# Kernel tuning notes

Hardware: AMD Instinct MI355X
Metric: run time of the kernel (lower is better)

## Reference

```python
import jax, jax.numpy as jnp
from jax import lax
import numpy as np

EPS = 1e-5

def _quant(w):
    # BitNet-style binarization: sign(w) scaled by mean(|w|), with STE (identity grad)
    alpha = jnp.mean(jnp.abs(w))
    wq = jnp.sign(w) * alpha
    return w + lax.stop_gradient(wq - w)

def _bn(x, gamma, beta, axes):
    mean = jnp.mean(x, axis=axes, keepdims=True)
    var = jnp.var(x, axis=axes, keepdims=True)
    shape = [1] * x.ndim
    shape[1] = x.shape[1]
    return (x - mean) * lax.rsqrt(var + EPS) * gamma.reshape(shape) + beta.reshape(shape)

def _conv(x, w):
    return lax.conv_general_dilated(x, w, window_strides=(1, 1), padding=((1, 1), (1, 1)),
                                    dimension_numbers=('NCHW', 'OIHW', 'NCHW'))

def _maxpool2(x):
    return lax.reduce_window(x, -jnp.inf, lax.max, (1, 1, 2, 2), (1, 1, 2, 2), 'VALID')

def setup_inputs() -> dict:
    key = jax.random.key(0)
    ks = jax.random.split(key, 5)
    return {
        'x': jax.random.normal(ks[0], (1024, 3, 32, 32), jnp.float32),
        'w1': jax.random.normal(ks[1], (64, 3, 3, 3), jnp.float32) * 0.1,
        'g1': jnp.ones((64,), jnp.float32), 'b1': jnp.zeros((64,), jnp.float32),
        'w2': jax.random.normal(ks[2], (128, 64, 3, 3), jnp.float32) * 0.05,
        'g2': jnp.ones((128,), jnp.float32), 'b2': jnp.zeros((128,), jnp.float32),
        'wfc1': jax.random.normal(ks[3], (256, 8192), jnp.float32) * 0.02,
        'g3': jnp.ones((256,), jnp.float32), 'b3': jnp.zeros((256,), jnp.float32),
        'wfc2': jax.random.normal(ks[4], (10, 256), jnp.float32) * 0.1,
    }

def reference(x, w1, g1, b1, w2, g2, b2, wfc1, g3, b3, wfc2):
    h = _conv(x, _quant(w1))                 # [B,64,32,32]
    h = _maxpool2(jax.nn.relu(_bn(h, g1, b1, (0, 2, 3))))  # [B,64,16,16]
    h = _conv(h, _quant(w2))                 # [B,128,16,16]
    h = _maxpool2(jax.nn.relu(_bn(h, g2, b2, (0, 2, 3))))  # [B,128,8,8]
    h = h.reshape(h.shape[0], -1)            # [B,8192]
    h = h @ _quant(wfc1).T                   # [B,256]
    h = jax.nn.relu(_bn(h, g3, b3, (0,)))
    return h @ _quant(wfc2).T                # [B,10]
```

## Files before the change

### kernel.cpp

```cpp
#include <hip/hip_runtime.h>
#include <stdint.h>

typedef unsigned short u16;
typedef unsigned int u32;
typedef __attribute__((ext_vector_type(8))) short s8v;
typedef __attribute__((ext_vector_type(4))) float f4v;
typedef __attribute__((ext_vector_type(8))) u16 u16x8;
typedef __attribute__((ext_vector_type(4))) u16 u16x4;

__device__ __forceinline__ float bf2f(u16 u){
  union { u32 i; float f; } v; v.i = ((u32)u) << 16; return v.f;
}
__device__ __forceinline__ u16 f2bf(float f){
  union { float f; u32 i; } v; v.f = f;
  u32 i = v.i;
  return (u16)((i + 0x7fffu + ((i >> 16) & 1u)) >> 16);
}
__device__ __forceinline__ float sgnf(float w){
  return (w > 0.f) ? 1.f : ((w < 0.f) ? -1.f : 0.f);
}
__device__ __forceinline__ u16 sgn_bf(float w){
  return (w > 0.f) ? (u16)0x3F80 : ((w < 0.f) ? (u16)0xBF80 : (u16)0);
}

#define GLL16(gaddr, laddr) __builtin_amdgcn_global_load_lds( \
    (const __attribute__((address_space(1))) void*)(gaddr),   \
    (__attribute__((address_space(3))) void*)(laddr), 16, 0, 0)


__global__ __launch_bounds__(256) void k_gen(const float* __restrict__ w1, const float* __restrict__ w2,
                                             const float* __restrict__ wfc2, const float* __restrict__ wfc1,
                                             u16* __restrict__ qw1b, u16* __restrict__ qw2b,
                                             float* __restrict__ qwfc2, u16* __restrict__ qfc1b,
                                             float* __restrict__ absum){
  __shared__ u16 tile[128*72];
  int t = threadIdx.x;
  if (blockIdx.x < 306){
    int i = blockIdx.x * 256 + t;
    if (i < 73728){
      int j = i & 7, lane = (i >> 3) & 63, fid = i >> 9;
      int s = fid >> 4, ks = (fid >> 3) & 1, nt = fid & 7;
      int co = (lane & 15)*8 + nt;
      int c_pos = ks*32 + (lane >> 4)*8 + j;
      int c6 = c_pos & 63;
      int c_orig = ((c6 & 3) << 4) + (c6 >> 2);
      qw2b[i] = sgn_bf(w2[((size_t)co*64 + c_orig)*9 + s]);
    } else if (i < 73728 + 2048){
      int i3 = i - 73728;
      int j = i3 & 7, lane = (i3 >> 3) & 63, nt = i3 >> 9;
      int co = nt*16 + (lane & 15);
      int k = (lane >> 4)*8 + j;
      qw1b[i3] = (k < 27) ? sgn_bf(w1[co*27 + k]) : (u16)0;
    } else {
      int i4 = i - (73728 + 2048);
      float wv = wfc2[i4];
      qwfc2[i4] = sgnf(wv);
      float av = fabsf(wv);
      #pragma unroll
      for (int off = 32; off > 0; off >>= 1) av += __shfl_xor(av, off);
      if ((t & 63) == 0) atomicAdd(absum + 3, av);
    }
  } else {
    int co = blockIdx.x - 306;
    const float4* src = (const float4*)(wfc1 + (size_t)co*8192);
    #pragma unroll
    for (int p = 0; p < 8; ++p){
      int k4 = t + p*256;
      float4 v = src[k4];
      int c = k4 >> 4, px = (k4 & 15)*4;
      u16* d = tile + c*72 + px;
      d[0] = sgn_bf(v.x); d[1] = sgn_bf(v.y); d[2] = sgn_bf(v.z); d[3] = sgn_bf(v.w);
    }
    __syncthreads();
    int co4 = co >> 4, co15 = co & 15;
    #pragma unroll
    for (int p = 0; p < 4; ++p){
      int m = t + p*256;
      int px = m >> 4, jj = m & 15;
      int kstep = px*4 + (jj >> 2), l16 = jj & 3;
      u16x8 o;
      #pragma unroll
      for (int u = 0; u < 8; ++u) o[u] = tile[(jj*8 + u)*72 + px];
      *(u16x8*)(qfc1b + ((size_t)(kstep*16 + co4)*512 + (l16*16 + co15)*8)) = o;
    }
  }
}

__global__ __launch_bounds__(256) void k_conv1m(const float* __restrict__ x, const u16* __restrict__ qw1b,
                                                u16* __restrict__ p1raw,
                                                float* __restrict__ gs, float* __restrict__ gq){
  __shared__ __align__(8) u16 xs[3*34*36];
  __shared__ float ls1[64], ls2[64];
  int n = blockIdx.x, t = threadIdx.x;
  if (t < 64){ ls1[t] = 0.f; ls2[t] = 0.f; }
  for (int i = t; i < 1836; i += 256) ((u32*)xs)[i] = 0u;
  __syncthreads();
  const float4* xg = (const float4*)(x + (size_t)n * 3072);
  for (int i = t; i < 768; i += 256){
    float4 v = xg[i];
    int ci = i >> 8, rem = i & 255, y = rem >> 3, xq = (rem & 7) * 4;
    int base = ci*1224 + (y+1)*36 + 2 + xq;
    *(u32*)(xs + base)     = (u32)f2bf(v.x) | ((u32)f2bf(v.y) << 16);
    *(u32*)(xs + base + 2) = (u32)f2bf(v.z) | ((u32)f2bf(v.w) << 16);
  }
  int w = t >> 6, lane = t & 63, l15 = lane & 15, q = lane >> 4;
  int koff[8]; u32 kmsk[8];
  #pragma unroll
  for (int j = 0; j < 8; ++j){
    int k = q*8 + j;
    int d9 = (k*57) >> 9;
    int r9 = k - d9*9;
    int d3 = (r9*11) >> 5;
    int r3 = r9 - d3*3;
    koff[j] = d9*1224 + d3*36 + r3;
    kmsk[j] = (k < 27) ? 0xffffu : 0u;
  }
  const s8v* bp = (const s8v*)qw1b;
  s8v bf[4];
  #pragma unroll
  for (int nt = 0; nt < 4; ++nt) bf[nt] = bp[nt*64 + lane];
  u16* p1img = p1raw + (size_t)n * 16384;
  float s1v[4], s2v[4];
  #pragma unroll
  for (int nt = 0; nt < 4; ++nt){ s1v[nt] = 0.f; s2v[nt] = 0.f; }
  __syncthreads();
  for (int chunk = 0; chunk < 4; ++chunk){
    #pragma unroll
    for (int i = 0; i < 4; ++i){
      int tl = w*4 + i;
      int r = tl*16 + l15;
      int g = (chunk*256 + r) >> 2, s = r & 3;
      int iy = 2*(g >> 4) + (s >> 1), ix = 2*(g & 15) + (s & 1);
      const u16* xb = xs + iy*36 + ix + 1;
      u32 pk2[4];
      #pragma unroll
      for (int kk = 0; kk < 4; ++kk){
        u32 lo = (u32)xb[koff[2*kk]]     & kmsk[2*kk];
        u32 hi = (u32)xb[koff[2*kk + 1]] & kmsk[2*kk + 1];
        pk2[kk] = lo | (hi << 16);
      }
      s8v av;
      ((u32*)&av)[0] = pk2[0]; ((u32*)&av)[1] = pk2[1];
      ((u32*)&av)[2] = pk2[2]; ((u32*)&av)[3] = pk2[3];
      int go = chunk*64 + tl*4 + q;
      u16x4 pk;
      #pragma unroll
      for (int nt = 0; nt < 4; ++nt){
        f4v c = (f4v)(0.0f);
        c = __builtin_amdgcn_mfma_f32_16x16x32_bf16(av, bf[nt], c, 0, 0, 0);
        s1v[nt] += c[0] + c[1] + c[2] + c[3];
        s2v[nt] += c[0]*c[0] + c[1]*c[1] + c[2]*c[2] + c[3]*c[3];
        float pm = fmaxf(fmaxf(c[0], c[1]), fmaxf(c[2], c[3]));
        pk[nt] = f2bf(pm);
      }
      *(u16x4*)(p1img + go*64 + l15*4) = pk;
    }
  }
  #pragma unroll
  for (int nt = 0; nt < 4; ++nt){
    s1v[nt] += __shfl_xor(s1v[nt], 16); s1v[nt] += __shfl_xor(s1v[nt], 32);
    s2v[nt] += __shfl_xor(s2v[nt], 16); s2v[nt] += __shfl_xor(s2v[nt], 32);
  }
  if (q == 0){
    #pragma unroll
    for (int nt = 0; nt < 4; ++nt){
      atomicAdd(&ls1[l15*4 + nt], s1v[nt]);
      atomicAdd(&ls2[l15*4 + nt], s2v[nt]);
    }
  }
  __syncthreads();
  if (t < 64){
    atomicAdd(gs + t, ls1[t]);
    atomicAdd(gq + t, ls2[t]);
  }
}

__global__ __launch_bounds__(512, 4) void k_conv2m(const u16* __restrict__ p1raw, const u16* __restrict__ qw2b,
                                                   const float* __restrict__ s1, const float* __restrict__ q1,
                                                   const float* __restrict__ g1, const float* __restrict__ b1,
                                                   u16* __restrict__ p2raw,
                                                   float* __restrict__ gs, float* __restrict__ gq){
  __shared__ __align__(16) u16 img[288*64];
  __shared__ __align__(16) u16 bstage[3][4096];
  int n = blockIdx.x, t = threadIdx.x;
  int c0 = (t & 7) * 8;
  float scv[8], biv[8];
  #pragma unroll
  for (int j = 0; j < 8; ++j){
    int cp = c0 + j;
    int corig = ((cp & 3) << 4) + (cp >> 2);
    float m = s1[cp] * (1.f/1048576.f);
    float var = q1[cp] * (1.f/1048576.f) - m*m;
    float sc = g1[corig] * rsqrtf(var + 1e-5f);
    scv[j] = sc; biv[j] = b1[corig] - m*sc;
  }
  if (t < 256){
    int cl = t >> 7, y = (t >> 3) & 15, unit = t & 7;
    int px = y*18 + cl*17;
    int su = unit ^ (px & 7);
    *(u16x8*)(img + px*64 + su*8) = (u16x8)(u16)0;
  }
  const u16* src = p1raw + (size_t)n * 16384;
  #pragma unroll
  for (int i = 0; i < 4; ++i){
    int id = i*512 + t;
    int p0 = id >> 3, unit = id & 7;
    int y = p0 >> 4, xq = p0 & 15;
    int px = y*18 + xq + 1;
    int su = unit ^ (px & 7);
    u16x8 v = *(const u16x8*)(src + id*8);
    u16x8 o;
    #pragma unroll
    for (int j = 0; j < 8; ++j)
      o[j] = f2bf(fmaxf(bf2f(v[j]) * scv[j] + biv[j], 0.f));
    *(u16x8*)(img + px*64 + su*8) = o;
  }
  int w = t >> 6, lane = t & 63, l15 = lane & 15, q = lane >> 4;
  int wr = w >> 1, wc = w & 1;
  const char* bsrc = (const char*)qw2b;
  {
    const char* g = bsrc + w*1024 + lane*16;
    GLL16(g, ((char*)bstage[0]) + w*1024);
  }
  __syncthreads();
  f4v acc[4][4];
  #pragma unroll
  for (int a = 0; a < 4; ++a)
    #pragma unroll
    for (int b = 0; b < 4; ++b) acc[a][b] = (f4v)(0.0f);
  for (int p = 0; p < 18; ++p){
    int s = p >> 1, ks = p & 1;
    int dy = s / 3, dx = s - dy*3;
    if (p < 17){
      const char* g = bsrc + (size_t)(p + 1)*8192 + w*1024 + lane*16;
      GLL16(g, ((char*)bstage[(p + 1) % 3]) + w*1024);
      asm volatile("s_waitcnt vmcnt(1)" ::: "memory");
    } else {
      asm volatile("s_waitcnt vmcnt(0)" ::: "memory");
    }
    __builtin_amdgcn_s_barrier();
    asm volatile("" ::: "memory");
    const u16* bb = bstage[p % 3];
    s8v bf[4];
    #pragma unroll
    for (int nt = 0; nt < 4; ++nt) bf[nt] = *(const s8v*)(bb + ((wc*4 + nt)*64 + lane)*8);
    __builtin_amdgcn_s_setprio(1);
    #pragma unroll
    for (int mt = 0; mt < 4; ++mt){
      int yv = wr*4 + mt + dy - 1;
      if (yv >= 0 && yv <= 15){
        int px = yv*18 + l15 + dx;
        int su = (ks*4 + q) ^ (px & 7);
        s8v av = *(const s8v*)(img + px*64 + su*8);
        #pragma unroll
        for (int nt = 0; nt < 4; ++nt)
          acc[mt][nt] = __builtin_amdgcn_mfma_f32_16x16x32_bf16(av, bf[nt], acc[mt][nt], 0, 0, 0);
      }
    }
    __builtin_amdgcn_s_setprio(0);
  }
  float s1v[4], s2v[4];
  #pragma unroll
  for (int nt = 0; nt < 4; ++nt){ s1v[nt] = 0.f; s2v[nt] = 0.f; }
  #pragma unroll
  for (int mp = 0; mp < 2; ++mp){
    #pragma unroll
    for (int rp = 0; rp < 2; ++rp){
      u16x4 pk;
      #pragma unroll
      for (int nt = 0; nt < 4; ++nt){
        float v0 = acc[2*mp][nt][2*rp];
        float v1 = acc[2*mp][nt][2*rp+1];
        float v2 = acc[2*mp+1][nt][2*rp];
        float v3 = acc[2*mp+1][nt][2*rp+1];
        s1v[nt] += v0 + v1 + v2 + v3;
        s2v[nt] += v0*v0 + v1*v1 + v2*v2 + v3*v3;
        pk[nt] = f2bf(fmaxf(fmaxf(v0, v1), fmaxf(v2, v3)));
      }
      int opx = (wr*2 + mp)*8 + (q*2 + rp);
      *(u16x4*)(p2raw + ((size_t)n*64 + opx)*128 + l15*8 + wc*4) = pk;
    }
  }
  #pragma unroll
  for (int nt = 0; nt < 4; ++nt){
    s1v[nt] += __shfl_xor(s1v[nt], 16); s1v[nt] += __shfl_xor(s1v[nt], 32);
    s2v[nt] += __shfl_xor(s2v[nt], 16); s2v[nt] += __shfl_xor(s2v[nt], 32);
  }
  __syncthreads();
  float* ls = (float*)img;
  if (t < 256) ls[t] = 0.f;
  __syncthreads();
  if (q == 0){
    #pragma unroll
    for (int nt = 0; nt < 4; ++nt){
      atomicAdd(&ls[l15*8 + wc*4 + nt], s1v[nt]);
      atomicAdd(&ls[128 + l15*8 + wc*4 + nt], s2v[nt]);
    }
  }
  __syncthreads();
  if (t < 128){ atomicAdd(gs + t, ls[t]); atomicAdd(gq + t, ls[128 + t]); }
}

__global__ __launch_bounds__(256) void k_fc1m(const u16* __restrict__ p2, const u16* __restrict__ qfc1b,
                                              const float* __restrict__ s2, const float* __restrict__ q2,
                                              const float* __restrict__ g2, const float* __restrict__ b2,
                                              float* __restrict__ h3p){
  int t = threadIdx.x;
  int bm = blockIdx.x, bn = blockIdx.y, kb = blockIdx.z;
  int w = t >> 6, lane = t & 63, l15 = lane & 15, q = lane >> 4;
  int wr = w >> 1, wc = w & 1;
  int rowbase = bm*32 + wr*16;
  int ntb = bn*8 + wc*4;
  const s8v* bp = (const s8v*)qfc1b;
  f4v acc[4];
  #pragma unroll
  for (int b = 0; b < 4; ++b) acc[b] = (f4v)(0.0f);
  #pragma unroll
  for (int ks4 = 0; ks4 < 4; ++ks4){
    int c0 = ks4*32 + q*8;
    float scv[8], biv[8];
    #pragma unroll
    for (int j = 0; j < 8; ++j){
      float m = s2[c0+j] * (1.f/262144.f);
      float var = q2[c0+j] * (1.f/262144.f) - m*m;
      float sc = g2[c0+j] * rsqrtf(var + 1e-5f);
      scv[j] = sc; biv[j] = b2[c0+j] - m*sc;
    }
    #pragma unroll 2
    for (int u = 0; u < 8; ++u){
      int ks = ks4 + u*4;
      int kst = kb*32 + ks;
      s8v bf[4];
      #pragma unroll
      for (int nt = 0; nt < 4; ++nt) bf[nt] = bp[(kst*16 + ntb + nt)*64 + lane];
      u16x8 araw = *(const u16x8*)(p2 + (size_t)(rowbase + l15)*8192 + kst*32 + q*8);
      s8v av;
      #pragma unroll
      for (int j = 0; j < 8; ++j){
        float f = fmaxf(bf2f(araw[j]) * scv[j] + biv[j], 0.f);
        ((u16*)&av)[j] = f2bf(f);
      }
      #pragma unroll
      for (int nt = 0; nt < 4; ++nt)
        acc[nt] = __builtin_amdgcn_mfma_f32_16x16x32_bf16(av, bf[nt], acc[nt], 0, 0, 0);
    }
  }
  float* dst = h3p + (size_t)kb * 262144;
  #pragma unroll
  for (int nt = 0; nt < 4; ++nt){
    int col = (ntb + nt)*16 + l15;
    #pragma unroll
    for (int r = 0; r < 4; ++r)
      dst[(size_t)(rowbase + q*4 + r)*256 + col] = acc[nt][r];
  }
}

__global__ __launch_bounds__(256) void k_fin3f(const float* __restrict__ h3p, float* __restrict__ h3,
                                               float* __restrict__ s3, float* __restrict__ q3){
  int jb = blockIdx.x, ns = blockIdx.y, t = threadIdx.x;
  int jj = t & 31, nn = t >> 5;
  int j = jb*32 + jj;
  float s1 = 0.f, s2 = 0.f;
  #pragma unroll
  for (int i = 0; i < 2; ++i){
    int n = ns*16 + i*8 + nn;
    float v = 0.f;
    #pragma unroll
    for (int kb = 0; kb < 8; ++kb) v += h3p[(size_t)kb*262144 + n*256 + j];
    h3[n*256 + j] = v;
    s1 += v; s2 += v*v;
  }
  __shared__ float l1[256], l2[256];
  l1[t] = s1; l2[t] = s2;
  __syncthreads();
  if (t < 32){
    float a = 0.f, b = 0.f;
    #pragma unroll
    for (int k = 0; k < 8; ++k){ a += l1[t+32*k]; b += l2[t+32*k]; }
    atomicAdd(s3 + jb*32 + t, a); atomicAdd(q3 + jb*32 + t, b);
  }
}

__global__ __launch_bounds__(256) void k_fc2(const float* __restrict__ h3, const float* __restrict__ qwfc2,
                                             const float* __restrict__ absum,
                                             const float* __restrict__ s3, const float* __restrict__ q3,
                                             const float* __restrict__ g3, const float* __restrict__ b3,
                                             float* __restrict__ out){
  int t = threadIdx.x;
  int n = blockIdx.x*4 + (t >> 6), lane = t & 63;
  float a[4];
  #pragma unroll
  for (int i = 0; i < 4; ++i){
    int j = lane + 64*i;
    float m = s3[j] * (1.f/1024.f);
    float var = q3[j] * (1.f/1024.f) - m*m;
    float sc = g3[j] * rsqrtf(var + 1e-5f);
    float v = h3[(size_t)n*256 + j] * sc + (b3[j] - m*sc);
    a[i] = fmaxf(v, 0.f);
  }
  float alpha = absum[3] * (1.f/2560.f);
  #pragma unroll
  for (int k = 0; k < 10; ++k){
    float p = 0.f;
    #pragma unroll
    for (int i = 0; i < 4; ++i) p += a[i] * qwfc2[k*256 + lane + 64*i];
    #pragma unroll
    for (int off = 32; off > 0; off >>= 1) p += __shfl_down(p, off);
    if (lane == 0) out[n*10 + k] = p * alpha;
  }
}

extern "C" void kernel_launch(void* const* d_in, const int* in_sizes, int n_in,
                              void* d_out, int out_size, void* d_ws, size_t ws_size,
                              hipStream_t stream){
  (void)in_sizes; (void)n_in; (void)out_size; (void)ws_size;
  const float* x    = (const float*)d_in[0];
  const float* w1   = (const float*)d_in[1];
  const float* g1   = (const float*)d_in[2];
  const float* b1   = (const float*)d_in[3];
  const float* w2   = (const float*)d_in[4];
  const float* g2   = (const float*)d_in[5];
  const float* b2   = (const float*)d_in[6];
  const float* wfc1 = (const float*)d_in[7];
  const float* g3   = (const float*)d_in[8];
  const float* b3   = (const float*)d_in[9];
  const float* wfc2 = (const float*)d_in[10];
  float* out = (float*)d_out;

  float* wsf = (float*)d_ws;
  char*  wsb = (char*)d_ws;
  float* absum = wsf;
  float* s1 = wsf + 16;   float* q1 = wsf + 80;
  float* s2 = wsf + 144;  float* q2 = wsf + 272;
  float* s3 = wsf + 1024; float* q3 = wsf + 1280;
  u16*   qw1b  = (u16*)(wsf + 4096);
  u16*   qw2b  = (u16*)(wsb + (64u << 10));
  float* qwfc2 = (float*)(wsb + (256u << 10));
  float* h3    = (float*)(wsb + (1ull << 20));
  u16*   qfc1b = (u16*)(wsb + (2ull << 20));
  u16*   p1t   = (u16*)(wsb + (8ull << 20) + 4096);
  u16*   p2    = (u16*)(wsb + (112ull << 20));
  float* h3p   = (float*)(wsb + (128ull << 20));

  hipMemsetAsync(wsf, 0, 2048 * sizeof(float), stream);
  k_gen<<<562, 256, 0, stream>>>(w1, w2, wfc2, wfc1, qw1b, qw2b, qwfc2, qfc1b, absum);
  k_conv1m<<<1024, 256, 0, stream>>>(x, qw1b, p1t, s1, q1);
  k_conv2m<<<1024, 512, 0, stream>>>(p1t, qw2b, s1, q1, g1, b1, p2, s2, q2);
  k_fc1m<<<dim3(32, 2, 8), 256, 0, stream>>>(p2, qfc1b, s2, q2, g2, b2, h3p);
  k_fin3f<<<dim3(8, 64), 256, 0, stream>>>(h3p, h3, s3, q3);
  k_fc2<<<256, 256, 0, stream>>>(h3, qwfc2, absum, s3, q3, g3, b3, out);
}
```

Measured before the change: 213.6 us.

## Double-buffer conv2 weights per tap and atomically reduce fc1 split-K partials

The conv2 inner loop now runs 9 iterations, one per 3x3 tap, each covering both K-halves. It double-buffers 16KB weight stages instead of triple-buffering 8KB stages, which halves the barriers and wait points. The fc1 split-K partial sums are now added with atomics directly into a zeroed h3 buffer, which k_gen clears. This removes the 8-way partial buffer and its reduction reads in k_fin3f. The cost is atomic contention on h3 and summation order that varies from run to run.

Result: faster. 209.3 us (-2.0%).

```diff
diff --git a/kernel.cpp b/kernel.cpp
--- a/kernel.cpp
+++ b/kernel.cpp
@@ -32,9 +32,12 @@
                                              const float* __restrict__ wfc2, const float* __restrict__ wfc1,
                                              u16* __restrict__ qw1b, u16* __restrict__ qw2b,
                                              float* __restrict__ qwfc2, u16* __restrict__ qfc1b,
-                                             float* __restrict__ absum){
+                                             float* __restrict__ absum, float* __restrict__ h3){
   __shared__ u16 tile[128*72];
   int t = threadIdx.x;
+  if (blockIdx.x < 256){
+    *(float4*)(h3 + ((size_t)blockIdx.x*256 + t)*4) = make_float4(0.f, 0.f, 0.f, 0.f);
+  }
   if (blockIdx.x < 306){
     int i = blockIdx.x * 256 + t;
     if (i < 73728){
@@ -181,7 +184,7 @@
                                                    u16* __restrict__ p2raw,
                                                    float* __restrict__ gs, float* __restrict__ gq){
   __shared__ __align__(16) u16 img[288*64];
-  __shared__ __align__(16) u16 bstage[3][4096];
+  __shared__ __align__(16) u16 bstage[2][8192];
   int n = blockIdx.x, t = threadIdx.x;
   int c0 = (t & 7) * 8;
   float scv[8], biv[8];
@@ -219,8 +222,9 @@
   int wr = w >> 1, wc = w & 1;
   const char* bsrc = (const char*)qw2b;
   {
-    const char* g = bsrc + w*1024 + lane*16;
-    GLL16(g, ((char*)bstage[0]) + w*1024);
+    const char* g = bsrc + w*2048 + lane*16;
+    char* l = ((char*)bstage[0]) + w*2048;
+    GLL16(g, l); GLL16(g + 1024, l + 1024);
   }
   __syncthreads();
   f4v acc[4][4];
@@ -228,36 +232,40 @@
   for (int a = 0; a < 4; ++a)
     #pragma unroll
     for (int b = 0; b < 4; ++b) acc[a][b] = (f4v)(0.0f);
-  for (int p = 0; p < 18; ++p){
-    int s = p >> 1, ks = p & 1;
-    int dy = s / 3, dx = s - dy*3;
-    if (p < 17){
-      const char* g = bsrc + (size_t)(p + 1)*8192 + w*1024 + lane*16;
-      GLL16(g, ((char*)bstage[(p + 1) % 3]) + w*1024);
-      asm volatile("s_waitcnt vmcnt(1)" ::: "memory");
-    } else {
-      asm volatile("s_waitcnt vmcnt(0)" ::: "memory");
-    }
-    __builtin_amdgcn_s_barrier();
-    asm volatile("" ::: "memory");
-    const u16* bb = bstage[p % 3];
-    s8v bf[4];
-    #pragma unroll
-    for (int nt = 0; nt < 4; ++nt) bf[nt] = *(const s8v*)(bb + ((wc*4 + nt)*64 + lane)*8);
+  for (int p = 0; p < 9; ++p){
+    int dy = p / 3, dx = p - dy*3;
+    if (p < 8){
+      const char* g = bsrc + (size_t)(p + 1)*16384 + w*2048 + lane*16;
+      char* l = ((char*)bstage[(p + 1) & 1]) + w*2048;
+      GLL16(g, l); GLL16(g + 1024, l + 1024);
+    }
+    const u16* bb = bstage[p & 1];
+    s8v bf[2][4];
+    #pragma unroll
+    for (int ks = 0; ks < 2; ++ks)
+      #pragma unroll
+      for (int nt = 0; nt < 4; ++nt)
+        bf[ks][nt] = *(const s8v*)(bb + ks*4096 + ((wc*4 + nt)*64 + lane)*8);
     __builtin_amdgcn_s_setprio(1);
     #pragma unroll
     for (int mt = 0; mt < 4; ++mt){
       int yv = wr*4 + mt + dy - 1;
       if (yv >= 0 && yv <= 15){
         int px = yv*18 + l15 + dx;
-        int su = (ks*4 + q) ^ (px & 7);
-        s8v av = *(const s8v*)(img + px*64 + su*8);
         #pragma unroll
-        for (int nt = 0; nt < 4; ++nt)
-          acc[mt][nt] = __builtin_amdgcn_mfma_f32_16x16x32_bf16(av, bf[nt], acc[mt][nt], 0, 0, 0);
+        for (int ks = 0; ks < 2; ++ks){
+          int su = (ks*4 + q) ^ (px & 7);
+          s8v av = *(const s8v*)(img + px*64 + su*8);
+          #pragma unroll
+          for (int nt = 0; nt < 4; ++nt)
+            acc[mt][nt] = __builtin_amdgcn_mfma_f32_16x16x32_bf16(av, bf[ks][nt], acc[mt][nt], 0, 0, 0);
+        }
       }
     }
     __builtin_amdgcn_s_setprio(0);
+    if (p < 8) asm volatile("s_waitcnt vmcnt(0)" ::: "memory");
+    __builtin_amdgcn_s_barrier();
+    asm volatile("" ::: "memory");
   }
   float s1v[4], s2v[4];
   #pragma unroll
@@ -304,7 +312,7 @@
 __global__ __launch_bounds__(256) void k_fc1m(const u16* __restrict__ p2, const u16* __restrict__ qfc1b,
                                               const float* __restrict__ s2, const float* __restrict__ q2,
                                               const float* __restrict__ g2, const float* __restrict__ b2,
-                                              float* __restrict__ h3p){
+                                              float* __restrict__ h3){
   int t = threadIdx.x;
   int bm = blockIdx.x, bn = blockIdx.y, kb = blockIdx.z;
   int w = t >> 6, lane = t & 63, l15 = lane & 15, q = lane >> 4;
@@ -345,29 +353,25 @@
         acc[nt] = __builtin_amdgcn_mfma_f32_16x16x32_bf16(av, bf[nt], acc[nt], 0, 0, 0);
     }
   }
-  float* dst = h3p + (size_t)kb * 262144;
   #pragma unroll
   for (int nt = 0; nt < 4; ++nt){
     int col = (ntb + nt)*16 + l15;
     #pragma unroll
     for (int r = 0; r < 4; ++r)
-      dst[(size_t)(rowbase + q*4 + r)*256 + col] = acc[nt][r];
-  }
-}
-
-__global__ __launch_bounds__(256) void k_fin3f(const float* __restrict__ h3p, float* __restrict__ h3,
+      atomicAdd(&h3[(size_t)(rowbase + q*4 + r)*256 + col], acc[nt][r]);
+  }
+}
+
+__global__ __launch_bounds__(256) void k_fin3f(const float* __restrict__ h3,
                                                float* __restrict__ s3, float* __restrict__ q3){
   int jb = blockIdx.x, ns = blockIdx.y, t = threadIdx.x;
   int jj = t & 31, nn = t >> 5;
   int j = jb*32 + jj;
   float s1 = 0.f, s2 = 0.f;
   #pragma unroll
-  for (int i = 0; i < 2; ++i){
-    int n = ns*16 + i*8 + nn;
-    float v = 0.f;
-    #pragma unroll
-    for (int kb = 0; kb < 8; ++kb) v += h3p[(size_t)kb*262144 + n*256 + j];
-    h3[n*256 + j] = v;
+  for (int i = 0; i < 4; ++i){
+    int n = ns*32 + i*8 + nn;
+    float v = h3[(size_t)n*256 + j];
     s1 += v; s2 += v*v;
   }
   __shared__ float l1[256], l2[256];
@@ -440,13 +444,12 @@
   u16*   qfc1b = (u16*)(wsb + (2ull << 20));
   u16*   p1t   = (u16*)(wsb + (8ull << 20) + 4096);
   u16*   p2    = (u16*)(wsb + (112ull << 20));
-  float* h3p   = (float*)(wsb + (128ull << 20));
 
   hipMemsetAsync(wsf, 0, 2048 * sizeof(float), stream);
-  k_gen<<<562, 256, 0, stream>>>(w1, w2, wfc2, wfc1, qw1b, qw2b, qwfc2, qfc1b, absum);
+  k_gen<<<562, 256, 0, stream>>>(w1, w2, wfc2, wfc1, qw1b, qw2b, qwfc2, qfc1b, absum, h3);
   k_conv1m<<<1024, 256, 0, stream>>>(x, qw1b, p1t, s1, q1);
   k_conv2m<<<1024, 512, 0, stream>>>(p1t, qw2b, s1, q1, g1, b1, p2, s2, q2);
-  k_fc1m<<<dim3(32, 2, 8), 256, 0, stream>>>(p2, qfc1b, s2, q2, g2, b2, h3p);
-  k_fin3f<<<dim3(8, 64), 256, 0, stream>>>(h3p, h3, s3, q3);
+  k_fc1m<<<dim3(32, 2, 8), 256, 0, stream>>>(p2, qfc1b, s2, q2, g2, b2, h3);
+  k_fin3f<<<dim3(8, 32), 256, 0, stream>>>(h3, s3, q3);
   k_fc2<<<256, 256, 0, stream>>>(h3, qwfc2, absum, s3, q3, g3, b3, out);
 }
```
